# Optimization experiments

Hardware: AMD Instinct MI355X
Metric: run time of the kernel (lower is better)

## Reference

```python
import jax, jax.numpy as jnp
import numpy as np

B, S, V, H = 64, 512, 128, 1024
TEMP = 1.0


def _lstm_layer(x_seq, W_ih, W_hh, b_ih, b_hh):
    """x_seq: (S, B, D_in) -> (S, B, H). PyTorch gate order: i, f, g, o."""
    Hh = W_hh.shape[1]
    Bb = x_seq.shape[1]
    # precompute input projections for all timesteps: (S, B, 4H)
    xW = jnp.einsum('sbd,gd->sbg', x_seq, W_ih) + (b_ih + b_hh)

    def step(carry, xw_t):
        h, c = carry
        gates = xw_t + h @ W_hh.T  # (B, 4H)
        i, f, g, o = jnp.split(gates, 4, axis=-1)
        i = jax.nn.sigmoid(i)
        f = jax.nn.sigmoid(f)
        g = jnp.tanh(g)
        o = jax.nn.sigmoid(o)
        c = f * c + i * g
        h = o * jnp.tanh(c)
        return (h, c), h

    h0 = jnp.zeros((Bb, Hh), dtype=x_seq.dtype)
    c0 = jnp.zeros((Bb, Hh), dtype=x_seq.dtype)
    _, hs = jax.lax.scan(step, (h0, c0), xW)
    return hs  # (S, B, H)


def setup_inputs() -> dict:
    key = jax.random.key(0)
    ks = jax.random.split(key, 11)
    s = 1.0 / np.sqrt(H)
    u = lambda k, shape: jax.random.uniform(k, shape, jnp.float32, -s, s)
    return {
        'x': jax.random.normal(ks[0], (B, S, V), jnp.float32),
        'W_ih0': u(ks[1], (4 * H, V)),
        'W_hh0': u(ks[2], (4 * H, H)),
        'b_ih0': u(ks[3], (4 * H,)),
        'b_hh0': u(ks[4], (4 * H,)),
        'W_ih1': u(ks[5], (4 * H, H)),
        'W_hh1': u(ks[6], (4 * H, H)),
        'b_ih1': u(ks[7], (4 * H,)),
        'b_hh1': u(ks[8], (4 * H,)),
        'W_fc': u(ks[9], (V, H)),
        'b_fc': u(ks[10], (V,)),
    }


def reference(x, W_ih0, W_hh0, b_ih0, b_hh0, W_ih1, W_hh1, b_ih1, b_hh1, W_fc, b_fc):
    xs = jnp.transpose(x, (1, 0, 2))  # (S, B, V)
    h1 = _lstm_layer(xs, W_ih0, W_hh0, b_ih0, b_hh0)   # (S, B, H)
    h2 = _lstm_layer(h1, W_ih1, W_hh1, b_ih1, b_hh1)   # (S, B, H)
    logits = jnp.einsum('sbh,vh->sbv', h2, W_fc) + b_fc  # (S, B, V)
    out = jax.nn.log_softmax(logits * TEMP, axis=-1)
    return jnp.transpose(out, (1, 0, 2))  # (B, S, V)
```

## Files before the change

### kernel.cpp

```cpp
#include <hip/hip_runtime.h>
#include <hip/hip_bf16.h>
#include <math.h>


#define S_LEN 512
#define B_SZ  64
#define V_SZ  128
#define H_SZ  1024
#define BH    65536
#define RING  32
#define SLOT  66560
#define FSTR  16
#define INVP  20
#define WSTR  1040

typedef unsigned short u16;
typedef unsigned short u16x8 __attribute__((ext_vector_type(8)));
typedef __bf16         bf16x8 __attribute__((ext_vector_type(8)));
typedef float          f32x4  __attribute__((ext_vector_type(4)));
typedef int            i32x4  __attribute__((ext_vector_type(4)));

__device__ __forceinline__ u16 f2bf(float f) {
    unsigned int u = __float_as_uint(f);
    u += 0x7fffu + ((u >> 16) & 1u);
    return (u16)(u >> 16);
}
__device__ __forceinline__ f32x4 mfma16(u16x8 a, u16x8 b, f32x4 c) {
    return __builtin_amdgcn_mfma_f32_16x16x32_bf16(
        __builtin_bit_cast(bf16x8, a), __builtin_bit_cast(bf16x8, b), c, 0, 0, 0);
}
__device__ __forceinline__ f32x4 mfma16(i32x4 a, u16x8 b, f32x4 c) {
    return __builtin_amdgcn_mfma_f32_16x16x32_bf16(
        __builtin_bit_cast(bf16x8, a), __builtin_bit_cast(bf16x8, b), c, 0, 0, 0);
}

__device__ __forceinline__ void ld_g(i32x4& d, const u16* p) {
    asm volatile("global_load_dwordx4 %0, %1, off" : "=v"(d) : "v"(p));
}
__device__ __forceinline__ void st_coh16(u16* p, u16x8 v) {
    i32x4 vv = __builtin_bit_cast(i32x4, v);
    asm volatile("global_store_dwordx4 %0, %1, off sc0 sc1" :: "v"(p), "v"(vv));
}
__device__ __forceinline__ int ld_flag(const int* p) {
    int v;
    asm volatile("global_load_dword %0, %1, off sc0 sc1\n\ts_waitcnt vmcnt(0)"
                 : "=v"(v) : "v"(p) : "memory");
    return v;
}
__device__ __forceinline__ void ld_flag_async(int& v, const int* p) {
    asm volatile("global_load_dword %0, %1, off sc0 sc1" : "=v"(v) : "v"(p));
}
__device__ __forceinline__ void flag_fence(int& v) {
    asm volatile("s_waitcnt vmcnt(0)" : "+v"(v) :: "memory");
}
__device__ __forceinline__ void st_flag(int* p, int v) {
    asm volatile("global_store_dword %0, %1, off sc0 sc1" :: "v"(p), "v"(v));
}
#define WAITV(n) asm volatile("s_waitcnt vmcnt(" #n ")" ::: "memory")
#define LGKM0    asm volatile("s_waitcnt lgkmcnt(0)" ::: "memory")
#define SCHEDB   __builtin_amdgcn_sched_barrier(0)

__device__ __forceinline__ void l2_acquire_inv() {
    __builtin_amdgcn_fence(__ATOMIC_ACQUIRE, "agent");
}

__global__ __launch_bounds__(256) void cvt_kernel(const float* __restrict__ s,
                                                  u16* __restrict__ d, int n)
{
    int i = (blockIdx.x * 256 + threadIdx.x) * 4;
    if (i >= n) return;
    float4 v = *(const float4*)(s + i);
    ushort4 o;
    o.x = f2bf(v.x); o.y = f2bf(v.y); o.z = f2bf(v.z); o.w = f2bf(v.w);
    *(ushort4*)(d + i) = o;
}

union SMemL {
    struct { u16 whh[64 * WSTR]; u16 wih[64 * 144]; u16 tr[4][384]; } l0;
    struct { u16 w[64 * WSTR]; u16 tr[4][384]; } l1;
    float lg[16][132];
};

__global__ __launch_bounds__(256, 1) void persist_kernel(
    const u16* __restrict__ xb,
    const u16* __restrict__ Wih0c, const u16* __restrict__ Whh0c,
    const u16* __restrict__ Wih1c, const u16* __restrict__ Whh1c,
    const u16* __restrict__ Wfcc,
    const float* __restrict__ bih0, const float* __restrict__ bhh0,
    const float* __restrict__ bih1, const float* __restrict__ bhh1,
    const float* __restrict__ bfc,
    u16* __restrict__ h0b, u16* __restrict__ h1b,
    int* __restrict__ flagL0, int* __restrict__ flagL1, int* __restrict__ flagFC,
    float* __restrict__ out)
{
    __shared__ SMemL sm;
    const int bid = blockIdx.x, tid = threadIdx.x;
    const int wave = tid >> 6, lane = tid & 63;
    const int l16 = lane & 15, kgi = lane >> 4, kg8 = kgi * 8;

    if (bid < 64) {
        const int j0 = bid * 16, jj = j0 + l16;
        for (int ch = tid; ch < 1024; ch += 256) {
            int row = ch >> 4, kc = ch & 15;
            int gr = (row >> 4) * H_SZ + j0 + (row & 15);
            *(u16x8*)&sm.l0.wih[row * 144 + kc * 8] =
                *(const u16x8*)(Wih0c + (size_t)gr * V_SZ + kc * 8);
        }
        for (int ch = tid; ch < 8192; ch += 256) {
            int row = ch >> 7, kc = ch & 127;
            int gr = (row >> 4) * H_SZ + j0 + (row & 15);
            *(u16x8*)&sm.l0.whh[row * WSTR + kc * 8] =
                *(const u16x8*)(Whh0c + (size_t)gr * H_SZ + kc * 8);
        }
        __syncthreads();

        const float bii = bih0[jj]            + bhh0[jj];
        const float bif = bih0[H_SZ + jj]     + bhh0[H_SZ + jj];
        const float big = bih0[2 * H_SZ + jj] + bhh0[2 * H_SZ + jj];
        const float bio = bih0[3 * H_SZ + jj] + bhh0[3 * H_SZ + jj];

        int whh_b[4], wih_b[4];
        #pragma unroll
        for (int g = 0; g < 4; ++g) {
            whh_b[g] = (g * 16 + l16) * WSTR + kg8;
            wih_b[g] = (g * 16 + l16) * 144 + kg8;
        }
        const int arow = wave * 16 + l16;
        const u16* xrow = xb + (size_t)arow * (S_LEN * V_SZ);
        u16* trw = sm.l0.tr[wave];
        float creg[4] = {0.f, 0.f, 0.f, 0.f};

        for (int t = 0; t < S_LEN; ++t) {
            i32x4 xq[4];
            {
                const u16* xp = xrow + (size_t)t * V_SZ + kg8;
                #pragma unroll
                for (int i = 0; i < 4; ++i) ld_g(xq[i], xp + i * 32);
            }
            const int* pA = nullptr; int tgtA = 0; int fvA = 0x7fffffff;
            if (tid < 64)                    { pA = flagL0 + tid * FSTR;        tgtA = t; }
            else if (tid < 192 && t >= RING) { pA = flagL1 + (tid - 64) * FSTR; tgtA = t - (RING - 1); }
            if (pA && tgtA > 0) ld_flag_async(fvA, pA);
            flag_fence(fvA);
            if (pA && tgtA > 0 && fvA < tgtA)
                while (ld_flag(pA) < tgtA) __builtin_amdgcn_s_sleep(2);
            __syncthreads();
            if (t >= INVP && (t % INVP) == 0) l2_acquire_inv();

            f32x4 acc[4][2] = {};
            auto ISSUE = [&](i32x4 (&buf)[8], const u16* base) {
                #pragma unroll
                for (int q = 0; q < 8; ++q) ld_g(buf[q], base + q * 32);
            };
            auto COMP = [&](i32x4 (&buf)[8], int k0) {
                #pragma unroll
                for (int q = 0; q < 8; ++q)
                    #pragma unroll
                    for (int g = 0; g < 4; ++g)
                        acc[g][q & 1] = mfma16(buf[q],
                            *(const u16x8*)&sm.l0.whh[whh_b[g] + (k0 + q) * 32],
                            acc[g][q & 1]);
            };
            const u16* aB = h0b + (size_t)((t - 1) & (RING - 1)) * SLOT
                          + (size_t)arow * H_SZ + kg8;
            i32x4 b0[8], b1[8], b2[8];
            ISSUE(b0, aB); ISSUE(b1, aB + 256); ISSUE(b2, aB + 512);
            SCHEDB;
            #pragma unroll
            for (int i = 0; i < 4; ++i)
                #pragma unroll
                for (int g = 0; g < 4; ++g)
                    acc[g][i & 1] = mfma16(xq[i],
                        *(const u16x8*)&sm.l0.wih[wih_b[g] + i * 32], acc[g][i & 1]);
            WAITV(16); SCHEDB; COMP(b0, 0);  ISSUE(b0, aB + 768);
            WAITV(16); SCHEDB; COMP(b1, 8);
            WAITV(8);  SCHEDB; COMP(b2, 16);
            WAITV(0);  SCHEDB; COMP(b0, 24);

            {
                u16* hout = h0b + (size_t)(t & (RING - 1)) * SLOT;
                #pragma unroll
                for (int r = 0; r < 4; ++r) {
                    const float ip = acc[0][0][r] + acc[0][1][r] + bii;
                    const float fp = acc[1][0][r] + acc[1][1][r] + bif;
                    const float gp = acc[2][0][r] + acc[2][1][r] + big;
                    const float op = acc[3][0][r] + acc[3][1][r] + bio;
                    const float iv = 1.f / (1.f + expf(-ip));
                    const float fv = 1.f / (1.f + expf(-fp));
                    const float gv = tanhf(gp);
                    const float ov = 1.f / (1.f + expf(-op));
                    const float cv = fv * creg[r] + iv * gv;
                    creg[r] = cv;
                    trw[(kgi * 4 + r) * 24 + l16] = f2bf(ov * tanhf(cv));
                }
                LGKM0; SCHEDB;
                if (lane < 32) {
                    int m = lane >> 1, jb = lane & 1;
                    u16x8 v = *(const u16x8*)&trw[m * 24 + jb * 8];
                    st_coh16(hout + (size_t)(wave * 16 + m) * H_SZ + j0 + jb * 8, v);
                }
                WAITV(0);
            }
            __syncthreads();
            if (tid == 0) st_flag(flagL0 + bid * FSTR, t + 1);
        }
        return;
    }

    if (bid < 192) {
        const int lb = bid - 64, j0 = lb * 8, jj2 = j0 + (l16 & 7);
        for (int ch = tid; ch < 8192; ch += 256) {
            int ldsrow = ch >> 7, kc = ch & 127;
            int region = ldsrow >> 5, rl = ldsrow & 31;
            int gr = (rl >> 3) * H_SZ + j0 + (rl & 7);
            const u16* src = (region ? Whh1c : Wih1c) + (size_t)gr * H_SZ + kc * 8;
            *(u16x8*)&sm.l1.w[ldsrow * WSTR + kc * 8] = *(const u16x8*)src;
        }
        __syncthreads();

        const float bii = bih1[jj2]            + bhh1[jj2];
        const float bif = bih1[H_SZ + jj2]     + bhh1[H_SZ + jj2];
        const float big = bih1[2 * H_SZ + jj2] + bhh1[2 * H_SZ + jj2];
        const float bio = bih1[3 * H_SZ + jj2] + bhh1[3 * H_SZ + jj2];
        const bool lo = (l16 < 8);

        int wrb[2][2];
        #pragma unroll
        for (int region = 0; region < 2; ++region)
            #pragma unroll
            for (int nt = 0; nt < 2; ++nt)
                wrb[region][nt] = (region * 32 + nt * 16 + l16) * WSTR + kg8;
        const int arow = wave * 16 + l16;
        u16* trw = sm.l1.tr[wave];
        float creg[4] = {0.f, 0.f, 0.f, 0.f};

        for (int t = 0; t < S_LEN; ++t) {
            const int* pA = nullptr; int tgtA = 0; int fvA = 0x7fffffff;
            if (tid < 64)                               { pA = flagL0 + tid * FSTR;         tgtA = t + 1; }
            else if (tid >= 192 && tid < 196 && t >= RING) { pA = flagFC + (tid - 192) * FSTR; tgtA = t - (RING - 1); }
            const int* pB = (tid < 128 && t > 0) ? (flagL1 + tid * FSTR) : nullptr;
            int fvB = 0x7fffffff;
            if (pA && tgtA > 0) ld_flag_async(fvA, pA);
            flag_fence(fvA);
            if (pA && tgtA > 0 && fvA < tgtA)
                while (ld_flag(pA) < tgtA) __builtin_amdgcn_s_sleep(2);
            __syncthreads();
            if (t >= INVP && (t % INVP) == 0) l2_acquire_inv();

            f32x4 acc[2][2] = {};
            auto ISSUE = [&](i32x4 (&buf)[8], const u16* base) {
                #pragma unroll
                for (int q = 0; q < 8; ++q) ld_g(buf[q], base + q * 32);
            };
            auto COMP = [&](i32x4 (&buf)[8], int region, int k0) {
                #pragma unroll
                for (int q = 0; q < 8; ++q)
                    #pragma unroll
                    for (int nt = 0; nt < 2; ++nt)
                        acc[nt][q & 1] = mfma16(buf[q],
                            *(const u16x8*)&sm.l1.w[wrb[region][nt] + (k0 + q) * 32],
                            acc[nt][q & 1]);
            };
            const u16* a1 = h0b + (size_t)(t & (RING - 1)) * SLOT + (size_t)arow * H_SZ + kg8;
            const u16* a2 = h1b + (size_t)((t - 1) & (RING - 1)) * SLOT + (size_t)arow * H_SZ + kg8;
            i32x4 b0[8], b1[8], b2[8];
            ISSUE(b0, a1); ISSUE(b1, a1 + 256); ISSUE(b2, a1 + 512);
            WAITV(16); SCHEDB; COMP(b0, 0, 0);  ISSUE(b0, a1 + 768);
            WAITV(16); SCHEDB; COMP(b1, 0, 8);
            WAITV(8);  SCHEDB; COMP(b2, 0, 16);
            if (pB) ld_flag_async(fvB, pB);
            WAITV(0);  SCHEDB; COMP(b0, 0, 24);
            flag_fence(fvB);
            if (pB && fvB < t)
                while (ld_flag(pB) < t) __builtin_amdgcn_s_sleep(2);
            __syncthreads();
            ISSUE(b0, a2); ISSUE(b1, a2 + 256); ISSUE(b2, a2 + 512);
            WAITV(16); SCHEDB; COMP(b0, 1, 0);  ISSUE(b0, a2 + 768);
            WAITV(16); SCHEDB; COMP(b1, 1, 8);
            WAITV(8);  SCHEDB; COMP(b2, 1, 16);
            WAITV(0);  SCHEDB; COMP(b0, 1, 24);

            {
                #pragma unroll
                for (int r = 0; r < 4; ++r) {
                    const float s0 = acc[0][0][r] + acc[0][1][r];
                    const float s1 = acc[1][0][r] + acc[1][1][r];
                    const float q0 = __shfl_xor(s0, 8);
                    const float q1 = __shfl_xor(s1, 8);
                    const float ip = (lo ? s0 : q0) + bii;
                    const float fp = (lo ? q0 : s0) + bif;
                    const float gp = (lo ? s1 : q1) + big;
                    const float op = (lo ? q1 : s1) + bio;
                    const float iv = 1.f / (1.f + expf(-ip));
                    const float fv = 1.f / (1.f + expf(-fp));
                    const float gv = tanhf(gp);
                    const float ov = 1.f / (1.f + expf(-op));
                    const float cv = fv * creg[r] + iv * gv;
                    creg[r] = cv;
                    if (lo) trw[(kgi * 4 + r) * 24 + (l16 & 7)] = f2bf(ov * tanhf(cv));
                }
                LGKM0; SCHEDB;
                if (lane < 16) {
                    int m = lane;
                    u16x8 v = *(const u16x8*)&trw[m * 24];
                    st_coh16(h1b + (size_t)(t & (RING - 1)) * SLOT
                             + (size_t)(wave * 16 + m) * H_SZ + j0, v);
                }
                WAITV(0);
            }
            __syncthreads();
            if (tid == 0) st_flag(flagL1 + lb * FSTR, t + 1);
        }
        return;
    }

    {
        const int fb = bid - 192, m0 = fb * 16;
        const u16* wp[2];
        #pragma unroll
        for (int nt = 0; nt < 2; ++nt)
            wp[nt] = Wfcc + (size_t)(wave * 32 + nt * 16 + l16) * H_SZ + kg8;

        for (int t = 0; t < S_LEN; ++t) {
            {
                const int* pA = (tid < 128) ? (flagL1 + tid * FSTR) : nullptr;
                int fvA = 0x7fffffff;
                if (pA) ld_flag_async(fvA, pA);
                flag_fence(fvA);
                if (pA && fvA < t + 1)
                    while (ld_flag(pA) < t + 1) __builtin_amdgcn_s_sleep(2);
                __syncthreads();
            }
            if (t >= INVP && (t % INVP) == 0) l2_acquire_inv();

            const u16* aB = h1b + (size_t)(t & (RING - 1)) * SLOT
                          + (size_t)(m0 + l16) * H_SZ + kg8;
            f32x4 acc[2][2] = {};
            i32x4 buf[8];
            WAITV(0);
            #pragma unroll
            for (int c = 0; c < 4; ++c) {
                #pragma unroll
                for (int q = 0; q < 8; ++q) ld_g(buf[q], aB + c * 256 + q * 32);
                WAITV(0); SCHEDB;
                #pragma unroll
                for (int q = 0; q < 8; ++q) {
                    #pragma unroll
                    for (int nt = 0; nt < 2; ++nt)
                        acc[nt][q & 1] = mfma16(buf[q],
                            *(const u16x8*)(wp[nt] + (c * 8 + q) * 32), acc[nt][q & 1]);
                }
            }
            #pragma unroll
            for (int nt = 0; nt < 2; ++nt)
                #pragma unroll
                for (int r = 0; r < 4; ++r) {
                    const int m = kgi * 4 + r, n = wave * 32 + nt * 16 + l16;
                    sm.lg[m][n] = acc[nt][0][r] + acc[nt][1][r] + bfc[n];
                }
            __syncthreads();
            const int row = tid >> 4, sub = tid & 15;
            float vals[8]; float mx = -1e30f;
            #pragma unroll
            for (int q = 0; q < 8; ++q) { vals[q] = sm.lg[row][sub * 8 + q]; mx = fmaxf(mx, vals[q]); }
            #pragma unroll
            for (int o = 1; o < 16; o <<= 1) mx = fmaxf(mx, __shfl_xor(mx, o));
            float se = 0.f;
            #pragma unroll
            for (int q = 0; q < 8; ++q) se += expf(vals[q] - mx);
            #pragma unroll
            for (int o = 1; o < 16; o <<= 1) se += __shfl_xor(se, o);
            const float ls = mx + logf(se);
            float* op = out + (size_t)(m0 + row) * (S_LEN * V_SZ) + (size_t)t * V_SZ + sub * 8;
            #pragma unroll
            for (int q = 0; q < 8; ++q) op[q] = vals[q] - ls;

            __syncthreads();
            if (tid == 0) st_flag(flagFC + fb * FSTR, t + 1);
        }
    }
}

extern "C" void kernel_launch(void* const* d_in, const int* in_sizes, int n_in,
                              void* d_out, int out_size, void* d_ws, size_t ws_size,
                              hipStream_t stream)
{
    const float* x    = (const float*)d_in[0];
    const float* Wih0 = (const float*)d_in[1];
    const float* Whh0 = (const float*)d_in[2];
    const float* bih0 = (const float*)d_in[3];
    const float* bhh0 = (const float*)d_in[4];
    const float* Wih1 = (const float*)d_in[5];
    const float* Whh1 = (const float*)d_in[6];
    const float* bih1 = (const float*)d_in[7];
    const float* bhh1 = (const float*)d_in[8];
    const float* Wfc  = (const float*)d_in[9];
    const float* bfc  = (const float*)d_in[10];
    float* out = (float*)d_out;

    u16* wih0 = (u16*)d_ws;
    u16* whh0 = wih0 + (size_t)4096 * 128;
    u16* wih1 = whh0 + (size_t)4096 * 1024;
    u16* whh1 = wih1 + (size_t)4096 * 1024;
    u16* wfc  = whh1 + (size_t)4096 * 1024;
    u16* xbuf = wfc  + (size_t)128 * 1024;
    u16* h0b  = xbuf + (size_t)B_SZ * S_LEN * V_SZ;
    u16* h1b  = h0b + (size_t)RING * SLOT;
    int* flags  = (int*)(h1b + (size_t)RING * SLOT);
    int* flagL0 = flags;
    int* flagL1 = flagL0 + 64 * FSTR;
    int* flagFC = flagL1 + 128 * FSTR;

    auto cvt = [&](const float* s, u16* d, int n) {
        cvt_kernel<<<(n / 4 + 255) / 256, 256, 0, stream>>>(s, d, n);
    };
    cvt(Wih0, wih0, 4096 * 128);
    cvt(Whh0, whh0, 4096 * 1024);
    cvt(Wih1, wih1, 4096 * 1024);
    cvt(Whh1, whh1, 4096 * 1024);
    cvt(Wfc,  wfc,  128 * 1024);
    cvt(x,    xbuf, B_SZ * S_LEN * V_SZ);
    hipMemsetAsync(h0b + (size_t)(RING - 1) * SLOT, 0, (size_t)BH * sizeof(u16), stream);
    hipMemsetAsync(h1b + (size_t)(RING - 1) * SLOT, 0, (size_t)BH * sizeof(u16), stream);
    hipMemsetAsync(flags, 0, (size_t)196 * FSTR * sizeof(int), stream);

    persist_kernel<<<196, 256, 0, stream>>>(
        xbuf, wih0, whh0, wih1, whh1, wfc,
        bih0, bhh0, bih1, bhh1, bfc,
        h0b, h1b, flagL0, flagL1, flagFC, out);
}
```

Measured before the change: 6.629 ms.

## Replace block-wide flag waits with per-wave polling and reorder layer-1 recurrence

Each wave now polls all producer flags itself with a wave-wide vote, replacing one thread per flag followed by __syncthreads. The layer-0 input projection is computed before the wait, and layer 1 now does its own recurrent h1 product first and waits for layer 0's output only afterwards. This removes block barriers from the critical recurrent chain and overlaps independent work with the inter-block dependency waits. In exchange every wave issues many more coherent flag loads, which adds memory traffic during polling.

```diff
diff --git a/kernel.cpp b/kernel.cpp
--- a/kernel.cpp
+++ b/kernel.cpp
@@ -34,7 +34,7 @@
         __builtin_bit_cast(bf16x8, a), __builtin_bit_cast(bf16x8, b), c, 0, 0, 0);
 }
 
-__device__ __forceinline__ void ld_g(i32x4& d, const u16* p) {
+__device__ __forceinline__ void ld_ca(i32x4& d, const u16* p) {
     asm volatile("global_load_dwordx4 %0, %1, off" : "=v"(d) : "v"(p));
 }
 __device__ __forceinline__ void st_coh16(u16* p, u16x8 v) {
@@ -47,14 +47,20 @@
                  : "=v"(v) : "v"(p) : "memory");
     return v;
 }
-__device__ __forceinline__ void ld_flag_async(int& v, const int* p) {
-    asm volatile("global_load_dword %0, %1, off sc0 sc1" : "=v"(v) : "v"(p));
-}
-__device__ __forceinline__ void flag_fence(int& v) {
-    asm volatile("s_waitcnt vmcnt(0)" : "+v"(v) :: "memory");
-}
 __device__ __forceinline__ void st_flag(int* p, int v) {
     asm volatile("global_store_dword %0, %1, off sc0 sc1" :: "v"(p), "v"(v));
+}
+__device__ __forceinline__ void poll3(const int* p0, int t0,
+                                      const int* p1, int t1,
+                                      const int* p2, int t2) {
+    for (;;) {
+        bool ok = true;
+        if (p0) ok = ok && (ld_flag(p0) >= t0);
+        if (p1) ok = ok && (ld_flag(p1) >= t1);
+        if (p2) ok = ok && (ld_flag(p2) >= t2);
+        if (__all(ok)) break;
+        __builtin_amdgcn_s_sleep(2);
+    }
 }
 #define WAITV(n) asm volatile("s_waitcnt vmcnt(" #n ")" ::: "memory")
 #define LGKM0    asm volatile("s_waitcnt lgkmcnt(0)" ::: "memory")
@@ -131,26 +137,28 @@
         float creg[4] = {0.f, 0.f, 0.f, 0.f};
 
         for (int t = 0; t < S_LEN; ++t) {
-            i32x4 xq[4];
+            f32x4 acc[4][2] = {};
             {
+                i32x4 xq[4];
                 const u16* xp = xrow + (size_t)t * V_SZ + kg8;
                 #pragma unroll
-                for (int i = 0; i < 4; ++i) ld_g(xq[i], xp + i * 32);
+                for (int i = 0; i < 4; ++i) ld_ca(xq[i], xp + i * 32);
+                WAITV(0); SCHEDB;
+                #pragma unroll
+                for (int i = 0; i < 4; ++i)
+                    #pragma unroll
+                    for (int g = 0; g < 4; ++g)
+                        acc[g][i & 1] = mfma16(xq[i],
+                            *(const u16x8*)&sm.l0.wih[wih_b[g] + i * 32], acc[g][i & 1]);
             }
-            const int* pA = nullptr; int tgtA = 0; int fvA = 0x7fffffff;
-            if (tid < 64)                    { pA = flagL0 + tid * FSTR;        tgtA = t; }
-            else if (tid < 192 && t >= RING) { pA = flagL1 + (tid - 64) * FSTR; tgtA = t - (RING - 1); }
-            if (pA && tgtA > 0) ld_flag_async(fvA, pA);
-            flag_fence(fvA);
-            if (pA && tgtA > 0 && fvA < tgtA)
-                while (ld_flag(pA) < tgtA) __builtin_amdgcn_s_sleep(2);
-            __syncthreads();
+            poll3((t >= 1)    ? flagL0 + lane * FSTR        : nullptr, t,
+                  (t >= RING) ? flagL1 + lane * FSTR        : nullptr, t - (RING - 1),
+                  (t >= RING) ? flagL1 + (64 + lane) * FSTR : nullptr, t - (RING - 1));
             if (t >= INVP && (t % INVP) == 0) l2_acquire_inv();
 
-            f32x4 acc[4][2] = {};
             auto ISSUE = [&](i32x4 (&buf)[8], const u16* base) {
                 #pragma unroll
-                for (int q = 0; q < 8; ++q) ld_g(buf[q], base + q * 32);
+                for (int q = 0; q < 8; ++q) ld_ca(buf[q], base + q * 32);
             };
             auto COMP = [&](i32x4 (&buf)[8], int k0) {
                 #pragma unroll
@@ -166,12 +174,6 @@
             i32x4 b0[8], b1[8], b2[8];
             ISSUE(b0, aB); ISSUE(b1, aB + 256); ISSUE(b2, aB + 512);
             SCHEDB;
-            #pragma unroll
-            for (int i = 0; i < 4; ++i)
-                #pragma unroll
-                for (int g = 0; g < 4; ++g)
-                    acc[g][i & 1] = mfma16(xq[i],
-                        *(const u16x8*)&sm.l0.wih[wih_b[g] + i * 32], acc[g][i & 1]);
             WAITV(16); SCHEDB; COMP(b0, 0);  ISSUE(b0, aB + 768);
             WAITV(16); SCHEDB; COMP(b1, 8);
             WAITV(8);  SCHEDB; COMP(b2, 16);
@@ -235,22 +237,15 @@
         float creg[4] = {0.f, 0.f, 0.f, 0.f};
 
         for (int t = 0; t < S_LEN; ++t) {
-            const int* pA = nullptr; int tgtA = 0; int fvA = 0x7fffffff;
-            if (tid < 64)                               { pA = flagL0 + tid * FSTR;         tgtA = t + 1; }
-            else if (tid >= 192 && tid < 196 && t >= RING) { pA = flagFC + (tid - 192) * FSTR; tgtA = t - (RING - 1); }
-            const int* pB = (tid < 128 && t > 0) ? (flagL1 + tid * FSTR) : nullptr;
-            int fvB = 0x7fffffff;
-            if (pA && tgtA > 0) ld_flag_async(fvA, pA);
-            flag_fence(fvA);
-            if (pA && tgtA > 0 && fvA < tgtA)
-                while (ld_flag(pA) < tgtA) __builtin_amdgcn_s_sleep(2);
-            __syncthreads();
+            poll3((t >= 1)    ? flagL1 + lane * FSTR        : nullptr, t,
+                  (t >= 1)    ? flagL1 + (64 + lane) * FSTR : nullptr, t,
+                  (t >= RING) ? flagFC + (lane & 3) * FSTR  : nullptr, t - (RING - 1));
             if (t >= INVP && (t % INVP) == 0) l2_acquire_inv();
 
             f32x4 acc[2][2] = {};
             auto ISSUE = [&](i32x4 (&buf)[8], const u16* base) {
                 #pragma unroll
-                for (int q = 0; q < 8; ++q) ld_g(buf[q], base + q * 32);
+                for (int q = 0; q < 8; ++q) ld_ca(buf[q], base + q * 32);
             };
             auto COMP = [&](i32x4 (&buf)[8], int region, int k0) {
                 #pragma unroll
@@ -261,24 +256,24 @@
                             *(const u16x8*)&sm.l1.w[wrb[region][nt] + (k0 + q) * 32],
                             acc[nt][q & 1]);
             };
-            const u16* a1 = h0b + (size_t)(t & (RING - 1)) * SLOT + (size_t)arow * H_SZ + kg8;
-            const u16* a2 = h1b + (size_t)((t - 1) & (RING - 1)) * SLOT + (size_t)arow * H_SZ + kg8;
+            const u16* a2 = h1b + (size_t)((t - 1) & (RING - 1)) * SLOT
+                          + (size_t)arow * H_SZ + kg8;
             i32x4 b0[8], b1[8], b2[8];
-            ISSUE(b0, a1); ISSUE(b1, a1 + 256); ISSUE(b2, a1 + 512);
-            WAITV(16); SCHEDB; COMP(b0, 0, 0);  ISSUE(b0, a1 + 768);
-            WAITV(16); SCHEDB; COMP(b1, 0, 8);
-            WAITV(8);  SCHEDB; COMP(b2, 0, 16);
-            if (pB) ld_flag_async(fvB, pB);
-            WAITV(0);  SCHEDB; COMP(b0, 0, 24);
-            flag_fence(fvB);
-            if (pB && fvB < t)
-                while (ld_flag(pB) < t) __builtin_amdgcn_s_sleep(2);
-            __syncthreads();
             ISSUE(b0, a2); ISSUE(b1, a2 + 256); ISSUE(b2, a2 + 512);
+            SCHEDB;
             WAITV(16); SCHEDB; COMP(b0, 1, 0);  ISSUE(b0, a2 + 768);
             WAITV(16); SCHEDB; COMP(b1, 1, 8);
             WAITV(8);  SCHEDB; COMP(b2, 1, 16);
             WAITV(0);  SCHEDB; COMP(b0, 1, 24);
+            poll3(flagL0 + lane * FSTR, t + 1, nullptr, 0, nullptr, 0);
+            const u16* a1 = h0b + (size_t)(t & (RING - 1)) * SLOT
+                          + (size_t)arow * H_SZ + kg8;
+            ISSUE(b0, a1); ISSUE(b1, a1 + 256); ISSUE(b2, a1 + 512);
+            SCHEDB;
+            WAITV(16); SCHEDB; COMP(b0, 0, 0);  ISSUE(b0, a1 + 768);
+            WAITV(16); SCHEDB; COMP(b1, 0, 8);
+            WAITV(8);  SCHEDB; COMP(b2, 0, 16);
+            WAITV(0);  SCHEDB; COMP(b0, 0, 24);
 
             {
                 #pragma unroll
@@ -322,26 +317,18 @@
             wp[nt] = Wfcc + (size_t)(wave * 32 + nt * 16 + l16) * H_SZ + kg8;
 
         for (int t = 0; t < S_LEN; ++t) {
-            {
-                const int* pA = (tid < 128) ? (flagL1 + tid * FSTR) : nullptr;
-                int fvA = 0x7fffffff;
-                if (pA) ld_flag_async(fvA, pA);
-                flag_fence(fvA);
-                if (pA && fvA < t + 1)
-                    while (ld_flag(pA) < t + 1) __builtin_amdgcn_s_sleep(2);
-                __syncthreads();
-            }
+            poll3(flagL1 + lane * FSTR, t + 1,
+                  flagL1 + (64 + lane) * FSTR, t + 1, nullptr, 0);
             if (t >= INVP && (t % INVP) == 0) l2_acquire_inv();
 
             const u16* aB = h1b + (size_t)(t & (RING - 1)) * SLOT
                           + (size_t)(m0 + l16) * H_SZ + kg8;
             f32x4 acc[2][2] = {};
             i32x4 buf[8];
-            WAITV(0);
             #pragma unroll
             for (int c = 0; c < 4; ++c) {
                 #pragma unroll
-                for (int q = 0; q < 8; ++q) ld_g(buf[q], aB + c * 256 + q * 32);
+                for (int q = 0; q < 8; ++q) ld_ca(buf[q], aB + c * 256 + q * 32);
                 WAITV(0); SCHEDB;
                 #pragma unroll
                 for (int q = 0; q < 8; ++q) {
```

Measured after the change: 6.778 ms. 1.02x slower.
